# Optimization experiments

Measured on AMD Instinct MI355X. Metric: run time of the kernel, lower is better.

The kernel has to match this reference:

```python
import jax, jax.numpy as jnp
import numpy as np

D_MODEL = 1024
H = 16
D_K = 64
D_V = 64
D_G = D_MODEL // H  # 64, trignometric embedding
WAVE_LEN = 1000.0
B = 8
N = 512


def box_relational_embedding(boxes, dim_g=D_G):
    # boxes: (b, n, 4) as (x_min, y_min, x_max, y_max)
    x_min, y_min, x_max, y_max = jnp.split(boxes, 4, axis=-1)  # each (b, n, 1)
    cx = (x_min + x_max) * 0.5
    cy = (y_min + y_max) * 0.5
    w = (x_max - x_min) + 1.0
    h = (y_max - y_min) + 1.0
    # pairwise log-ratios, (b, n, n)
    delta_x = jnp.log(jnp.clip(jnp.abs((cx - jnp.swapaxes(cx, 1, 2)) / w), 1e-3, None))
    delta_y = jnp.log(jnp.clip(jnp.abs((cy - jnp.swapaxes(cy, 1, 2)) / h), 1e-3, None))
    delta_w = jnp.log(w / jnp.swapaxes(w, 1, 2))
    delta_h = jnp.log(h / jnp.swapaxes(h, 1, 2))
    pos = jnp.stack([delta_x, delta_y, delta_w, delta_h], axis=-1)  # (b, n, n, 4)
    n_freq = dim_g // 8
    feat_range = jnp.arange(n_freq, dtype=jnp.float32)
    dim_mat = 1.0 / (WAVE_LEN ** (feat_range / n_freq))  # (n_freq,)
    mul = (100.0 * pos)[..., None] * dim_mat  # (b, n, n, 4, n_freq)
    b, n = pos.shape[0], pos.shape[1]
    mul = mul.reshape(b, n, n, 4 * n_freq)
    return jnp.concatenate([jnp.sin(mul), jnp.cos(mul)], axis=-1)  # (b, n, n, dim_g)


def setup_inputs() -> dict:
    key = jax.random.key(0)
    ks = jax.random.split(key, 12)
    s = 0.02
    inp = {
        "queries": jax.random.normal(ks[0], (B, N, D_MODEL), jnp.float32),
        "keys": jax.random.normal(ks[1], (B, N, D_MODEL), jnp.float32),
        "values": jax.random.normal(ks[2], (B, N, D_MODEL), jnp.float32),
        "boxes": jax.random.uniform(ks[3], (B, N, 4), jnp.float32),
        "Wq": jax.random.normal(ks[4], (H * D_K, D_MODEL), jnp.float32) * s,
        "bq": jnp.zeros((H * D_K,), jnp.float32),
        "Wk": jax.random.normal(ks[5], (H * D_K, D_MODEL), jnp.float32) * s,
        "bk": jnp.zeros((H * D_K,), jnp.float32),
        "Wv": jax.random.normal(ks[6], (H * D_V, D_MODEL), jnp.float32) * s,
        "bv": jnp.zeros((H * D_V,), jnp.float32),
        "Wo": jax.random.normal(ks[7], (D_MODEL, H * D_V), jnp.float32) * s,
        "bo": jnp.zeros((D_MODEL,), jnp.float32),
        "Wg": jax.random.normal(ks[8], (H, D_G), jnp.float32) * s,  # h separate Linear(d_g,1) stacked
        "bg": jnp.zeros((H,), jnp.float32),
    }
    return inp


def reference(queries, keys, values, boxes, Wq, bq, Wk, bk, Wv, bv, Wo, bo, Wg, bg):
    b, nq, _ = queries.shape
    nk = keys.shape[1]
    # per-head geometry bias
    emb = box_relational_embedding(boxes)  # (b, nk, nk, D_G)
    g = jax.nn.relu(jnp.einsum('bnmd,hd->bhnm', emb, Wg) + bg[None, :, None, None])
    # QKV projections, split heads
    q = (queries @ Wq.T + bq).reshape(b, nq, H, D_K).transpose(0, 2, 1, 3)  # (b,h,nq,dk)
    k = (keys @ Wk.T + bk).reshape(b, nk, H, D_K).transpose(0, 2, 1, 3)    # (b,h,nk,dk)
    v = (values @ Wv.T + bv).reshape(b, nk, H, D_V).transpose(0, 2, 1, 3)  # (b,h,nk,dv)
    a = jnp.einsum('bhqd,bhkd->bhqk', q, k) / jnp.sqrt(jnp.float32(D_K))
    mn = jax.nn.softmax(jnp.log(jnp.clip(g, 1e-6, None)) + a, axis=-1)
    out = jnp.einsum('bhqk,bhkd->bqhd', mn, v).reshape(b, nq, H * D_V)
    return out @ Wo.T + bo
```

## Files before the change

kernel.cpp:

```cpp
#include <hip/hip_runtime.h>
#include <hip/hip_bf16.h>
#include <hip/hip_fp16.h>

typedef __attribute__((ext_vector_type(8))) short bf16x8;
typedef __attribute__((ext_vector_type(8))) _Float16 f16x8;
typedef __attribute__((ext_vector_type(4))) float f32x4;

__device__ __forceinline__ short f2bf(float x) {
    unsigned u = __builtin_bit_cast(unsigned, x);
    u += 0x7fffu + ((u >> 16) & 1u);
    return (short)(u >> 16);
}

__device__ __forceinline__ void load_lds16(const void* g, void* l) {
    __builtin_amdgcn_global_load_lds((const __attribute__((address_space(1))) unsigned int*)g,
                                     (__attribute__((address_space(3))) unsigned int*)l, 16, 0, 0);
}

__global__ void convert_qkv(const float* __restrict__ q, const float* __restrict__ k,
                            const float* __restrict__ v, short* __restrict__ qo,
                            short* __restrict__ ko, short* __restrict__ vo) {
    int i = blockIdx.x * 256 + threadIdx.x;
    const float* s = blockIdx.y == 0 ? q : blockIdx.y == 1 ? k : v;
    short* d = blockIdx.y == 0 ? qo : blockIdx.y == 1 ? ko : vo;
    float4 val = reinterpret_cast<const float4*>(s)[i];
    short4 o; o.x = f2bf(val.x); o.y = f2bf(val.y); o.z = f2bf(val.z); o.w = f2bf(val.w);
    reinterpret_cast<short4*>(d)[i] = o;
}

__global__ void convert_w4(const float* __restrict__ w0, const float* __restrict__ w1,
                           const float* __restrict__ w2, const float* __restrict__ w3,
                           short* __restrict__ o0, short* __restrict__ o1,
                           short* __restrict__ o2, short* __restrict__ o3) {
    int i = blockIdx.x * 256 + threadIdx.x;
    const float* s = blockIdx.y == 0 ? w0 : blockIdx.y == 1 ? w1 : blockIdx.y == 2 ? w2 : w3;
    short* d = blockIdx.y == 0 ? o0 : blockIdx.y == 1 ? o1 : blockIdx.y == 2 ? o2 : o3;
    float4 val = reinterpret_cast<const float4*>(s)[i];
    short4 o; o.x = f2bf(val.x); o.y = f2bf(val.y); o.z = f2bf(val.z); o.w = f2bf(val.w);
    reinterpret_cast<short4*>(d)[i] = o;
}

__global__ void convert_f32_f16(const float* __restrict__ src, _Float16* __restrict__ dst, int n) {
    int i = blockIdx.x * blockDim.x + threadIdx.x;
    if (i < n) dst[i] = (_Float16)src[i];
}

__global__ void geom_kernel2(const float* __restrict__ boxes, const _Float16* __restrict__ Wgh,
                             const float* __restrict__ bg, __half* __restrict__ G) {
    const int tid = threadIdx.x;
    const int wave = tid >> 6, lane = tid & 63, quad = lane >> 4, l16 = lane & 15;
    const int m0 = blockIdx.x * 64;
    const int n = blockIdx.y;
    const int b = blockIdx.z;

    __shared__ __align__(16) _Float16 feat[4][16][72];
    __shared__ __align__(16) _Float16 gbuf[16][68];

    const int p = lane >> 2, c = lane & 3;
    const int m = m0 + wave * 16 + p;

    float4 bn = reinterpret_cast<const float4*>(boxes)[b * 512 + n];
    float4 bm = reinterpret_cast<const float4*>(boxes)[b * 512 + m];
    float cxn = (bn.x + bn.z) * 0.5f, cyn = (bn.y + bn.w) * 0.5f;
    float wn = bn.z - bn.x + 1.0f, hn = bn.w - bn.y + 1.0f;
    float cxm = (bm.x + bm.z) * 0.5f, cym = (bm.y + bm.w) * 0.5f;
    float wm = bm.z - bm.x + 1.0f, hm = bm.w - bm.y + 1.0f;

    float r;
    if (c == 0)      r = fmaxf(fabsf((cxn - cxm) / wn), 1e-3f);
    else if (c == 1) r = fmaxf(fabsf((cyn - cym) / hn), 1e-3f);
    else if (c == 2) r = wn / wm;
    else             r = hn / hm;
    float pos = __logf(r) * 100.0f;

    const float dm[8] = {1.0f, 0.42169651f, 0.17782794f, 0.07498942f,
                         0.03162278f, 0.01333521f, 0.00562341f, 0.00237137f};
    f16x8 sv8, cv8;
    #pragma unroll
    for (int f = 0; f < 8; ++f) {
        float th = pos * dm[f];
        sv8[f] = (_Float16)__sinf(th);
        cv8[f] = (_Float16)__cosf(th);
    }
    *(f16x8*)&feat[wave][p][c * 8]      = sv8;
    *(f16x8*)&feat[wave][p][32 + c * 8] = cv8;

    __syncthreads();

    f16x8 a0 = *(const f16x8*)&feat[wave][l16][quad * 8];
    f16x8 a1 = *(const f16x8*)&feat[wave][l16][32 + quad * 8];
    f16x8 b0 = *(const f16x8*)(Wgh + l16 * 64 + quad * 8);
    f16x8 b1 = *(const f16x8*)(Wgh + l16 * 64 + 32 + quad * 8);
    f32x4 acc = (f32x4){0.f, 0.f, 0.f, 0.f};
    acc = __builtin_amdgcn_mfma_f32_16x16x32_f16(a0, b0, acc, 0, 0, 0);
    acc = __builtin_amdgcn_mfma_f32_16x16x32_f16(a1, b1, acc, 0, 0, 0);

    float bgv = bg[l16];
    #pragma unroll
    for (int rr = 0; rr < 4; ++rr) {
        float g = fmaxf(acc[rr] + bgv, 1e-6f);
        gbuf[l16][wave * 16 + quad * 4 + rr] = (_Float16)g;
    }
    __syncthreads();

    const int h = tid >> 4, seg = tid & 15;
    ushort4 v = *(const ushort4*)&gbuf[h][seg * 4];
    *(ushort4*)&G[((long)((b * 16 + h) * 512 + n)) * 512 + m0 + seg * 4] = v;
}

__global__ __launch_bounds__(256, 2)
void proj_all(const short* __restrict__ qkbf, const short* __restrict__ wqkb,
              const short* __restrict__ wvb, const short* __restrict__ vbf,
              const float* __restrict__ bq, const float* __restrict__ bk,
              const float* __restrict__ bv,
              short* __restrict__ QKh, _Float16* __restrict__ Vt) {
    __shared__ __align__(16) short As[4096];
    __shared__ __align__(16) short Bs[4096];
    const int tid = threadIdx.x;
    const int wave = tid >> 6, lane = tid & 63, quad = lane >> 4, l16 = lane & 15;
    const int bid = blockIdx.x;

    const short *Ap, *Bp;
    int m0, n0, z = 0;
    bool isV = bid >= 512;
    if (!isV) {
        z = bid >> 8;
        int t = bid & 255;
        n0 = (t & 7) * 128; m0 = (t >> 3) * 128;
        Ap = qkbf + (long)z * 4194304 + (long)m0 * 1024;
        Bp = wqkb + (long)z * 1048576 + (long)n0 * 1024;
    } else {
        int t = bid - 512;
        n0 = (t & 31) * 128; m0 = (t >> 5) * 128;
        Ap = wvb + (long)m0 * 1024;
        Bp = vbf + (long)n0 * 1024;
    }

    f32x4 acc[4][4];
    #pragma unroll
    for (int mg = 0; mg < 4; ++mg)
        #pragma unroll
        for (int ng = 0; ng < 4; ++ng) acc[mg][ng] = (f32x4){0.f, 0.f, 0.f, 0.f};

    const int r0 = tid >> 2, kk = (tid & 3) * 8;
    const short* ga0 = Ap + (long)r0 * 1024 + kk;
    const short* ga1 = Ap + (long)(64 + r0) * 1024 + kk;
    const short* gb0 = Bp + (long)r0 * 1024 + kk;
    const short* gb1 = Bp + (long)(64 + r0) * 1024 + kk;
    short* la0 = As + wave * 512;
    short* la1 = As + 2048 + wave * 512;
    short* lb0 = Bs + wave * 512;
    short* lb1 = Bs + 2048 + wave * 512;

    const int mw = (wave >> 1) * 64, nw = (wave & 1) * 64;

    for (int k0 = 0; k0 < 1024; k0 += 32) {
        load_lds16(ga0 + k0, la0);
        load_lds16(ga1 + k0, la1);
        load_lds16(gb0 + k0, lb0);
        load_lds16(gb1 + k0, lb1);
        __syncthreads();
        bf16x8 a[4], bb[4];
        #pragma unroll
        for (int g = 0; g < 4; ++g) {
            a[g]  = *(const bf16x8*)&As[(mw + g * 16 + l16) * 32 + quad * 8];
            bb[g] = *(const bf16x8*)&Bs[(nw + g * 16 + l16) * 32 + quad * 8];
        }
        #pragma unroll
        for (int mg = 0; mg < 4; ++mg)
            #pragma unroll
            for (int ng = 0; ng < 4; ++ng)
                acc[mg][ng] = __builtin_amdgcn_mfma_f32_16x16x32_bf16(a[mg], bb[ng], acc[mg][ng], 0, 0, 0);
        __syncthreads();
    }

    #pragma unroll
    for (int mg = 0; mg < 4; ++mg)
        #pragma unroll
        for (int ng = 0; ng < 4; ++ng)
            #pragma unroll
            for (int r = 0; r < 4; ++r) {
                int row = m0 + mw + mg * 16 + quad * 4 + r;
                int col = n0 + nw + ng * 16 + l16;
                if (!isV) {
                    float v = acc[mg][ng][r] + (z ? bk[col] : bq[col]);
                    QKh[(long)z * 4194304 + (long)row * 1024 + col] = f2bf(v);
                } else {
                    float v = acc[mg][ng][r] + bv[row];
                    int bcol = col >> 9, lc = col & 511;
                    Vt[(long)bcol * 524288 + (long)row * 512 + lc] = (_Float16)v;
                }
            }
}

__global__ __launch_bounds__(512, 4)
void flash_attn5(const short* __restrict__ Q, const short* __restrict__ Kh,
                 const _Float16* __restrict__ Vt, const __half* __restrict__ G,
                 short* __restrict__ O) {
    const int tid = threadIdx.x;
    const int wave = tid >> 6, lane = tid & 63, quad = lane >> 4, l16 = lane & 15;
    const int wq = wave & 3, half = wave >> 2;
    const int qt = blockIdx.x, h = blockIdx.y, b = blockIdx.z;

    __shared__ __align__(16) _Float16 Pbuf[8][16][72];
    __shared__ __align__(16) float Obuf[4][16][64];
    __shared__ float Rbuf[4][16];

    const int qrow = qt * 64 + wq * 16;
    const long qoff = ((long)(b * 512 + qrow + l16)) * 1024 + h * 64 + quad * 8;
    bf16x8 aq0 = *(const bf16x8*)(Q + qoff);
    bf16x8 aq1 = *(const bf16x8*)(Q + qoff + 32);

    const _Float16* Gq = (const _Float16*)G +
        ((long)((b * 16 + h) * 512 + qrow + l16)) * 512 + half * 256;
    const short* Kb = Kh + ((long)(b * 512 + half * 256)) * 1024 + h * 64 + quad * 8;

    f16x8 gA = *(const f16x8*)(Gq + quad * 8);
    f16x8 gB = *(const f16x8*)(Gq + 32 + quad * 8);
    bf16x8 kf0[4], kf1[4];
    #pragma unroll
    for (int nk = 0; nk < 4; ++nk) {
        const long ko = (long)(nk * 16 + l16) * 1024;
        kf0[nk] = *(const bf16x8*)(Kb + ko);
        kf1[nk] = *(const bf16x8*)(Kb + ko + 32);
    }

    f32x4 oacc[4];
    #pragma unroll
    for (int r = 0; r < 4; ++r) oacc[r] = (f32x4){0.f, 0.f, 0.f, 0.f};
    float rs = 0.f;

    #pragma unroll
    for (int i = 0; i < 4; ++i) {
        const int kt = half * 4 + i;
        f32x4 sc[4];
        #pragma unroll
        for (int nk = 0; nk < 4; ++nk) {
            f32x4 s = (f32x4){0.f, 0.f, 0.f, 0.f};
            s = __builtin_amdgcn_mfma_f32_16x16x32_bf16(aq0, kf0[nk], s, 0, 0, 0);
            s = __builtin_amdgcn_mfma_f32_16x16x32_bf16(aq1, kf1[nk], s, 0, 0, 0);
            sc[nk] = s;
        }
        f16x8 gA1, gB1;
        if (i < 3) {
            #pragma unroll
            for (int nk = 0; nk < 4; ++nk) {
                const long ko = (long)((i + 1) * 64 + nk * 16 + l16) * 1024;
                kf0[nk] = *(const bf16x8*)(Kb + ko);
                kf1[nk] = *(const bf16x8*)(Kb + ko + 32);
            }
            gA1 = *(const f16x8*)(Gq + (i + 1) * 64 + quad * 8);
            gB1 = *(const f16x8*)(Gq + (i + 1) * 64 + 32 + quad * 8);
        }
        #pragma unroll
        for (int nk = 0; nk < 4; ++nk)
            #pragma unroll
            for (int r = 0; r < 4; ++r)
                Pbuf[wave][quad * 4 + r][nk * 16 + l16] = (_Float16)__expf(sc[nk][r] * 0.125f);
        f16x8 ep0 = *(const f16x8*)&Pbuf[wave][l16][quad * 8];
        f16x8 ep1 = *(const f16x8*)&Pbuf[wave][l16][32 + quad * 8];
        f16x8 gp0 = ep0 * gA;
        f16x8 gp1 = ep1 * gB;
        float part = 0.f;
        #pragma unroll
        for (int j = 0; j < 8; ++j) part += (float)gp0[j] + (float)gp1[j];
        rs += part;
        #pragma unroll
        for (int n4 = 0; n4 < 4; ++n4) {
            const long voff = ((long)(b * 1024 + h * 64 + n4 * 16 + l16)) * 512 + kt * 64 + quad * 8;
            f16x8 bv0 = *(const f16x8*)(Vt + voff);
            f16x8 bv1 = *(const f16x8*)(Vt + voff + 32);
            oacc[n4] = __builtin_amdgcn_mfma_f32_16x16x32_f16(gp0, bv0, oacc[n4], 0, 0, 0);
            oacc[n4] = __builtin_amdgcn_mfma_f32_16x16x32_f16(gp1, bv1, oacc[n4], 0, 0, 0);
        }
        gA = gA1; gB = gB1;
    }

    rs += __shfl_xor(rs, 16);
    rs += __shfl_xor(rs, 32);

    if (half == 1) {
        if (lane < 16) Rbuf[wq][l16] = rs;
        #pragma unroll
        for (int n4 = 0; n4 < 4; ++n4)
            #pragma unroll
            for (int r = 0; r < 4; ++r)
                Obuf[wq][quad * 4 + r][n4 * 16 + l16] = oacc[n4][r];
    }
    __syncthreads();
    if (half == 0) {
        rs += Rbuf[wq][l16];
        float li[4];
        #pragma unroll
        for (int r = 0; r < 4; ++r) li[r] = __shfl(rs, quad * 4 + r);
        #pragma unroll
        for (int n4 = 0; n4 < 4; ++n4)
            #pragma unroll
            for (int r = 0; r < 4; ++r) {
                float o = (oacc[n4][r] + Obuf[wq][quad * 4 + r][n4 * 16 + l16]) / li[r];
                O[((long)(b * 512 + qrow + quad * 4 + r)) * 1024 + h * 64 + n4 * 16 + l16] = f2bf(o);
            }
    }
}

__global__ __launch_bounds__(256, 2)
void gemm_out(const short* __restrict__ Hd, const short* __restrict__ wob,
              const float* __restrict__ bo, float* __restrict__ out) {
    __shared__ __align__(16) short As[4096];
    __shared__ __align__(16) short Bs[4096];
    const int tid = threadIdx.x;
    const int wave = tid >> 6, lane = tid & 63, quad = lane >> 4, l16 = lane & 15;
    const int m0 = blockIdx.y * 128, n0 = blockIdx.x * 128;
    const short* Ap = Hd + (long)m0 * 1024;
    const short* Bp = wob + (long)n0 * 1024;

    f32x4 acc[4][4];
    #pragma unroll
    for (int mg = 0; mg < 4; ++mg)
        #pragma unroll
        for (int ng = 0; ng < 4; ++ng) acc[mg][ng] = (f32x4){0.f, 0.f, 0.f, 0.f};

    const int r0 = tid >> 2, kk = (tid & 3) * 8;
    const short* ga0 = Ap + (long)r0 * 1024 + kk;
    const short* ga1 = Ap + (long)(64 + r0) * 1024 + kk;
    const short* gb0 = Bp + (long)r0 * 1024 + kk;
    const short* gb1 = Bp + (long)(64 + r0) * 1024 + kk;
    short* la0 = As + wave * 512;
    short* la1 = As + 2048 + wave * 512;
    short* lb0 = Bs + wave * 512;
    short* lb1 = Bs + 2048 + wave * 512;

    const int mw = (wave >> 1) * 64, nw = (wave & 1) * 64;

    for (int k0 = 0; k0 < 1024; k0 += 32) {
        load_lds16(ga0 + k0, la0);
        load_lds16(ga1 + k0, la1);
        load_lds16(gb0 + k0, lb0);
        load_lds16(gb1 + k0, lb1);
        __syncthreads();
        bf16x8 a[4], bb[4];
        #pragma unroll
        for (int g = 0; g < 4; ++g) {
            a[g]  = *(const bf16x8*)&As[(mw + g * 16 + l16) * 32 + quad * 8];
            bb[g] = *(const bf16x8*)&Bs[(nw + g * 16 + l16) * 32 + quad * 8];
        }
        #pragma unroll
        for (int mg = 0; mg < 4; ++mg)
            #pragma unroll
            for (int ng = 0; ng < 4; ++ng)
                acc[mg][ng] = __builtin_amdgcn_mfma_f32_16x16x32_bf16(a[mg], bb[ng], acc[mg][ng], 0, 0, 0);
        __syncthreads();
    }

    #pragma unroll
    for (int mg = 0; mg < 4; ++mg)
        #pragma unroll
        for (int ng = 0; ng < 4; ++ng)
            #pragma unroll
            for (int r = 0; r < 4; ++r) {
                int row = m0 + mw + mg * 16 + quad * 4 + r;
                int col = n0 + nw + ng * 16 + l16;
                out[(long)row * 1024 + col] = acc[mg][ng][r] + bo[col];
            }
}

extern "C" void kernel_launch(void* const* d_in, const int* in_sizes, int n_in,
                              void* d_out, int out_size, void* d_ws, size_t ws_size,
                              hipStream_t stream) {
    const float* queries = (const float*)d_in[0];
    const float* keys    = (const float*)d_in[1];
    const float* values  = (const float*)d_in[2];
    const float* boxes   = (const float*)d_in[3];
    const float* bq = (const float*)d_in[5];
    const float* bk = (const float*)d_in[7];
    const float* bv = (const float*)d_in[9];
    const float* bo = (const float*)d_in[11];
    const float* Wg = (const float*)d_in[12];
    const float* bg = (const float*)d_in[13];

    char* ws = (char*)d_ws;
    short* qbf = (short*)(ws + 0);
    short* kbf = (short*)(ws + 8388608);
    short* vbf = (short*)(ws + 16777216);
    short* wqb = (short*)(ws + 25165824);
    short* wkb = (short*)(ws + 27262976);
    short* wvb = (short*)(ws + 29360128);
    short* wob = (short*)(ws + 31457280);
    short* Qh  = (short*)(ws + 33554432);
    _Float16* Vt = (_Float16*)(ws + 50331648);
    short* Hd  = (short*)(ws + 58720256);
    __half* G  = (__half*)(ws + 67108864);
    _Float16* Wgh = (_Float16*)(ws + 33554432);

    convert_qkv<<<dim3(4096, 3), 256, 0, stream>>>(queries, keys, values, qbf, kbf, vbf);
    convert_w4<<<dim3(1024, 4), 256, 0, stream>>>((const float*)d_in[4], (const float*)d_in[6],
                                                  (const float*)d_in[8], (const float*)d_in[10],
                                                  wqb, wkb, wvb, wob);
    convert_f32_f16<<<4, 256, 0, stream>>>(Wg, Wgh, 1024);

    geom_kernel2<<<dim3(8, 512, 8), 256, 0, stream>>>(boxes, Wgh, bg, G);

    proj_all<<<768, 256, 0, stream>>>(qbf, wqb, wvb, vbf, bq, bk, bv, Qh, Vt);

    flash_attn5<<<dim3(8, 16, 8), 512, 0, stream>>>(Qh, Qh + 4194304, Vt, G, Hd);

    gemm_out<<<dim3(8, 32), 256, 0, stream>>>(Hd, wob, bo, (float*)d_out);
}
```

Before: 306.0 us.

## Stage K, V and G tiles through LDS and drop key-split in attention

The attention kernel goes from 512 threads, with the keys split across two wave halves and a final LDS reduction, to 256 threads that walk all 8 key tiles sequentially. Each K, V and geometry tile is loaded cooperatively into shared memory and shared by the four waves, so the per-wave redundant global loads of K and V go away. The cost is two block barriers per tile and no register prefetch of the next tile, so global latency is exposed unless occupancy hides it.

```diff
diff --git a/kernel.cpp b/kernel.cpp
--- a/kernel.cpp
+++ b/kernel.cpp
@@ -5,6 +5,7 @@
 typedef __attribute__((ext_vector_type(8))) short bf16x8;
 typedef __attribute__((ext_vector_type(8))) _Float16 f16x8;
 typedef __attribute__((ext_vector_type(4))) float f32x4;
+typedef __attribute__((ext_vector_type(8))) short short8;
 
 __device__ __forceinline__ short f2bf(float x) {
     unsigned u = __builtin_bit_cast(unsigned, x);
@@ -193,64 +194,60 @@
             }
 }
 
-__global__ __launch_bounds__(512, 4)
-void flash_attn5(const short* __restrict__ Q, const short* __restrict__ Kh,
+__global__ __launch_bounds__(256, 4)
+void flash_attn6(const short* __restrict__ Q, const short* __restrict__ Kh,
                  const _Float16* __restrict__ Vt, const __half* __restrict__ G,
                  short* __restrict__ O) {
     const int tid = threadIdx.x;
     const int wave = tid >> 6, lane = tid & 63, quad = lane >> 4, l16 = lane & 15;
-    const int wq = wave & 3, half = wave >> 2;
     const int qt = blockIdx.x, h = blockIdx.y, b = blockIdx.z;
 
-    __shared__ __align__(16) _Float16 Pbuf[8][16][72];
-    __shared__ __align__(16) float Obuf[4][16][64];
-    __shared__ float Rbuf[4][16];
-
-    const int qrow = qt * 64 + wq * 16;
+    __shared__ __align__(16) short    Ks[64][72];
+    __shared__ __align__(16) _Float16 Vs[64][72];
+    __shared__ __align__(16) _Float16 Gs[64][72];
+    __shared__ __align__(16) _Float16 Pbuf[4][16][72];
+
+    const int qrow = qt * 64 + wave * 16;
     const long qoff = ((long)(b * 512 + qrow + l16)) * 1024 + h * 64 + quad * 8;
     bf16x8 aq0 = *(const bf16x8*)(Q + qoff);
     bf16x8 aq1 = *(const bf16x8*)(Q + qoff + 32);
 
-    const _Float16* Gq = (const _Float16*)G +
-        ((long)((b * 16 + h) * 512 + qrow + l16)) * 512 + half * 256;
-    const short* Kb = Kh + ((long)(b * 512 + half * 256)) * 1024 + h * 64 + quad * 8;
-
-    f16x8 gA = *(const f16x8*)(Gq + quad * 8);
-    f16x8 gB = *(const f16x8*)(Gq + 32 + quad * 8);
-    bf16x8 kf0[4], kf1[4];
-    #pragma unroll
-    for (int nk = 0; nk < 4; ++nk) {
-        const long ko = (long)(nk * 16 + l16) * 1024;
-        kf0[nk] = *(const bf16x8*)(Kb + ko);
-        kf1[nk] = *(const bf16x8*)(Kb + ko + 32);
-    }
+    const int sr0 = tid >> 3,        sc0 = (tid & 7) * 8;
+    const int sr1 = (tid + 256) >> 3, sc1 = ((tid + 256) & 7) * 8;
+    const short* Kbase = Kh + (long)(b * 512) * 1024 + h * 64;
+    const _Float16* Vbase = Vt + (long)b * 524288 + (long)(h * 64) * 512;
+    const _Float16* Gbase = (const _Float16*)G + ((long)((b * 16 + h) * 512 + qt * 64)) * 512;
 
     f32x4 oacc[4];
     #pragma unroll
     for (int r = 0; r < 4; ++r) oacc[r] = (f32x4){0.f, 0.f, 0.f, 0.f};
     float rs = 0.f;
 
-    #pragma unroll
-    for (int i = 0; i < 4; ++i) {
-        const int kt = half * 4 + i;
+    for (int kt = 0; kt < 8; ++kt) {
+        __syncthreads();
+        short8 k0 = *(const short8*)(Kbase + (long)(kt * 64 + sr0) * 1024 + sc0);
+        short8 k1 = *(const short8*)(Kbase + (long)(kt * 64 + sr1) * 1024 + sc1);
+        short8 v0 = *(const short8*)(Vbase + (long)sr0 * 512 + kt * 64 + sc0);
+        short8 v1 = *(const short8*)(Vbase + (long)sr1 * 512 + kt * 64 + sc1);
+        short8 g0 = *(const short8*)(Gbase + (long)sr0 * 512 + kt * 64 + sc0);
+        short8 g1 = *(const short8*)(Gbase + (long)sr1 * 512 + kt * 64 + sc1);
+        *(short8*)&Ks[sr0][sc0] = k0;
+        *(short8*)&Ks[sr1][sc1] = k1;
+        *(short8*)&Vs[sr0][sc0] = v0;
+        *(short8*)&Vs[sr1][sc1] = v1;
+        *(short8*)&Gs[sr0][sc0] = g0;
+        *(short8*)&Gs[sr1][sc1] = g1;
+        __syncthreads();
+
         f32x4 sc[4];
         #pragma unroll
         for (int nk = 0; nk < 4; ++nk) {
+            bf16x8 bk0 = *(const bf16x8*)&Ks[nk * 16 + l16][quad * 8];
+            bf16x8 bk1 = *(const bf16x8*)&Ks[nk * 16 + l16][32 + quad * 8];
             f32x4 s = (f32x4){0.f, 0.f, 0.f, 0.f};
-            s = __builtin_amdgcn_mfma_f32_16x16x32_bf16(aq0, kf0[nk], s, 0, 0, 0);
-            s = __builtin_amdgcn_mfma_f32_16x16x32_bf16(aq1, kf1[nk], s, 0, 0, 0);
+            s = __builtin_amdgcn_mfma_f32_16x16x32_bf16(aq0, bk0, s, 0, 0, 0);
+            s = __builtin_amdgcn_mfma_f32_16x16x32_bf16(aq1, bk1, s, 0, 0, 0);
             sc[nk] = s;
-        }
-        f16x8 gA1, gB1;
-        if (i < 3) {
-            #pragma unroll
-            for (int nk = 0; nk < 4; ++nk) {
-                const long ko = (long)((i + 1) * 64 + nk * 16 + l16) * 1024;
-                kf0[nk] = *(const bf16x8*)(Kb + ko);
-                kf1[nk] = *(const bf16x8*)(Kb + ko + 32);
-            }
-            gA1 = *(const f16x8*)(Gq + (i + 1) * 64 + quad * 8);
-            gB1 = *(const f16x8*)(Gq + (i + 1) * 64 + 32 + quad * 8);
         }
         #pragma unroll
         for (int nk = 0; nk < 4; ++nk)
@@ -259,6 +256,8 @@
                 Pbuf[wave][quad * 4 + r][nk * 16 + l16] = (_Float16)__expf(sc[nk][r] * 0.125f);
         f16x8 ep0 = *(const f16x8*)&Pbuf[wave][l16][quad * 8];
         f16x8 ep1 = *(const f16x8*)&Pbuf[wave][l16][32 + quad * 8];
+        f16x8 gA = *(const f16x8*)&Gs[wave * 16 + l16][quad * 8];
+        f16x8 gB = *(const f16x8*)&Gs[wave * 16 + l16][32 + quad * 8];
         f16x8 gp0 = ep0 * gA;
         f16x8 gp1 = ep1 * gB;
         float part = 0.f;
@@ -267,40 +266,26 @@
         rs += part;
         #pragma unroll
         for (int n4 = 0; n4 < 4; ++n4) {
-            const long voff = ((long)(b * 1024 + h * 64 + n4 * 16 + l16)) * 512 + kt * 64 + quad * 8;
-            f16x8 bv0 = *(const f16x8*)(Vt + voff);
-            f16x8 bv1 = *(const f16x8*)(Vt + voff + 32);
+            f16x8 bv0 = *(const f16x8*)&Vs[n4 * 16 + l16][quad * 8];
+            f16x8 bv1 = *(const f16x8*)&Vs[n4 * 16 + l16][32 + quad * 8];
             oacc[n4] = __builtin_amdgcn_mfma_f32_16x16x32_f16(gp0, bv0, oacc[n4], 0, 0, 0);
             oacc[n4] = __builtin_amdgcn_mfma_f32_16x16x32_f16(gp1, bv1, oacc[n4], 0, 0, 0);
         }
-        gA = gA1; gB = gB1;
     }
 
     rs += __shfl_xor(rs, 16);
     rs += __shfl_xor(rs, 32);
-
-    if (half == 1) {
-        if (lane < 16) Rbuf[wq][l16] = rs;
-        #pragma unroll
-        for (int n4 = 0; n4 < 4; ++n4)
-            #pragma unroll
-            for (int r = 0; r < 4; ++r)
-                Obuf[wq][quad * 4 + r][n4 * 16 + l16] = oacc[n4][r];
-    }
-    __syncthreads();
-    if (half == 0) {
-        rs += Rbuf[wq][l16];
-        float li[4];
-        #pragma unroll
-        for (int r = 0; r < 4; ++r) li[r] = __shfl(rs, quad * 4 + r);
-        #pragma unroll
-        for (int n4 = 0; n4 < 4; ++n4)
-            #pragma unroll
-            for (int r = 0; r < 4; ++r) {
-                float o = (oacc[n4][r] + Obuf[wq][quad * 4 + r][n4 * 16 + l16]) / li[r];
-                O[((long)(b * 512 + qrow + quad * 4 + r)) * 1024 + h * 64 + n4 * 16 + l16] = f2bf(o);
-            }
-    }
+    float li[4];
+    #pragma unroll
+    for (int r = 0; r < 4; ++r) li[r] = __shfl(rs, quad * 4 + r);
+
+    #pragma unroll
+    for (int n4 = 0; n4 < 4; ++n4)
+        #pragma unroll
+        for (int r = 0; r < 4; ++r) {
+            float o = oacc[n4][r] / li[r];
+            O[((long)(b * 512 + qrow + quad * 4 + r)) * 1024 + h * 64 + n4 * 16 + l16] = f2bf(o);
+        }
 }
 
 __global__ __launch_bounds__(256, 2)
@@ -402,7 +387,7 @@
 
     proj_all<<<768, 256, 0, stream>>>(qbf, wqb, wvb, vbf, bq, bk, bv, Qh, Vt);
 
-    flash_attn5<<<dim3(8, 16, 8), 512, 0, stream>>>(Qh, Qh + 4194304, Vt, G, Hd);
+    flash_attn6<<<dim3(8, 16, 8), 256, 0, stream>>>(Qh, Qh + 4194304, Vt, G, Hd);
 
     gemm_out<<<dim3(8, 32), 256, 0, stream>>>(Hd, wob, bo, (float*)d_out);
 }
```

New measurement: 280.5 us. -8.3%, faster.
